# Kernel optimization log

Hardware: AMD Instinct MI355X
Metric: run time of the kernel (lower is better)

## Reference

```python
import jax, jax.numpy as jnp
import numpy as np

EMBED_DIM = 512
NUM_HEADS = 8
HEAD_DIM = EMBED_DIM // NUM_HEADS
B, S = 2, 4096


def setup_inputs() -> dict:
    key = jax.random.key(0)
    ks = jax.random.split(key, 5)
    scale = 1.0 / np.sqrt(EMBED_DIM)
    x = jax.random.normal(ks[0], (B, S, EMBED_DIM), dtype=jnp.float32)
    Wq = jax.random.normal(ks[1], (EMBED_DIM, EMBED_DIM), dtype=jnp.float32) * scale
    Wk = jax.random.normal(ks[2], (EMBED_DIM, EMBED_DIM), dtype=jnp.float32) * scale
    Wv = jax.random.normal(ks[3], (EMBED_DIM, EMBED_DIM), dtype=jnp.float32) * scale
    Wo = jax.random.normal(ks[4], (EMBED_DIM, EMBED_DIM), dtype=jnp.float32) * scale
    z = jnp.zeros((EMBED_DIM,), dtype=jnp.float32)
    return {"x": x, "Wq": Wq, "bq": z, "Wk": Wk, "bk": z, "Wv": Wv, "bv": z, "Wo": Wo, "bo": z}


def _split_heads(t):
    # [B, S, E] -> [B, H, S, Dh]
    b, s, _ = t.shape
    return t.reshape(b, s, NUM_HEADS, HEAD_DIM).transpose(0, 2, 1, 3)


def reference(x, Wq, bq, Wk, bk, Wv, bv, Wo, bo):
    q = _split_heads(x @ Wq + bq)
    k = _split_heads(x @ Wk + bk)
    v = _split_heads(x @ Wv + bv)
    # scaled dot-product attention; scale by sqrt(d_head) as in source
    scores = jnp.einsum("bhqd,bhkd->bhqk", q, k) / jnp.sqrt(jnp.float32(HEAD_DIM))
    weights = jax.nn.softmax(scores, axis=-1)
    attn = jnp.einsum("bhqk,bhkd->bhqd", weights, v)
    concat = attn.transpose(0, 2, 1, 3).reshape(x.shape[0], x.shape[1], EMBED_DIM)
    return concat @ Wo + bo
```

## Files before the change

kernel.cpp:

```cpp
#include <hip/hip_runtime.h>
#include <stdint.h>


typedef __bf16 bf16_t;
typedef bf16_t bf16x8 __attribute__((ext_vector_type(8)));
typedef float f32x4 __attribute__((ext_vector_type(4)));
typedef unsigned short u16;
typedef unsigned int u32;

__device__ __forceinline__ u16 f2bf(float f) {
  return __builtin_bit_cast(u16, (bf16_t)f);
}

__device__ __forceinline__ void gll16(const void* g, void* l) {
  __builtin_amdgcn_global_load_lds((__attribute__((address_space(1))) void*)(void*)(g),
                                   (__attribute__((address_space(3))) void*)(l), 16, 0, 0);
}

__device__ __forceinline__ float fexp2(float x) {
  float r; asm("v_exp_f32 %0, %1" : "=v"(r) : "v"(x)); return r;
}
__device__ __forceinline__ u32 cvtpk(float lo, float hi) {
  u32 r; asm("v_cvt_pk_bf16_f32 %0, %1, %2" : "=v"(r) : "v"(lo), "v"(hi)); return r;
}

__global__ void k_convert(const float* __restrict__ x, u16* __restrict__ xb, int n4) {
  int i = blockIdx.x * blockDim.x + threadIdx.x;
  if (i >= n4) return;
  float4 v = ((const float4*)x)[i];
  ushort4 o;
  o.x = f2bf(v.x); o.y = f2bf(v.y); o.z = f2bf(v.z); o.w = f2bf(v.w);
  ((ushort4*)xb)[i] = o;
}

__global__ void k_transposeW(const float* __restrict__ W0, const float* __restrict__ W1,
                             const float* __restrict__ W2, const float* __restrict__ W3,
                             u16* __restrict__ Wt) {
  __shared__ float tile[64][65];
  const float* W = (blockIdx.z == 0) ? W0 : (blockIdx.z == 1) ? W1 : (blockIdx.z == 2) ? W2 : W3;
  u16* out = Wt + (size_t)blockIdx.z * (512 * 512);
  int k0 = blockIdx.x * 64, n0 = blockIdx.y * 64;
  int t = threadIdx.x;
#pragma unroll
  for (int i = 0; i < 16; ++i) {
    int idx = i * 256 + t;
    int r = idx >> 6, c = idx & 63;
    tile[r][c] = W[(size_t)(k0 + r) * 512 + n0 + c];
  }
  __syncthreads();
#pragma unroll
  for (int i = 0; i < 16; ++i) {
    int idx = i * 256 + t;
    int n = idx >> 6, k = idx & 63;
    out[(size_t)(n0 + n) * 512 + k0 + k] = f2bf(tile[k][n]);
  }
}

__device__ __forceinline__ void gemm_core(const u16* __restrict__ A, const u16* __restrict__ Bt,
                                          int m0, int n0, uint8_t* lds, f32x4 (&acc)[4][4]) {
  int t = threadIdx.x;
  int lane = t & 63;
  int wid = t >> 6;
  int l15 = lane & 15, hib = (lane >> 4) * 16;
  int wm = wid >> 1, wn = wid & 1;
  const uint8_t* Ab = (const uint8_t*)A + (size_t)m0 * 1024;
  const uint8_t* Bb = (const uint8_t*)Bt + (size_t)n0 * 1024;
  for (int kk = 0; kk < 8; ++kk) {
    __syncthreads();
    int kof = kk * 128;
#pragma unroll
    for (int r = 0; r < 4; ++r) {
      int L = r * 4096 + t * 16;
      int row = L >> 7;
      int colU = (L & 127) ^ ((row & 7) << 4);
      gll16(Ab + (size_t)row * 1024 + kof + colU, lds + L);
      gll16(Bb + (size_t)row * 1024 + kof + colU, lds + 16384 + L);
    }
    __syncthreads();
#pragma unroll
    for (int ks = 0; ks < 2; ++ks) {
      bf16x8 af[4], bfr[4];
#pragma unroll
      for (int mi = 0; mi < 4; ++mi) {
        int row = wm * 64 + mi * 16 + l15;
        af[mi] = *(const bf16x8*)(lds + row * 128 + ((ks * 64 + hib) ^ ((row & 7) << 4)));
      }
#pragma unroll
      for (int ni = 0; ni < 4; ++ni) {
        int row = wn * 64 + ni * 16 + l15;
        bfr[ni] = *(const bf16x8*)(lds + 16384 + row * 128 + ((ks * 64 + hib) ^ ((row & 7) << 4)));
      }
#pragma unroll
      for (int mi = 0; mi < 4; ++mi)
#pragma unroll
        for (int ni = 0; ni < 4; ++ni)
          acc[mi][ni] = __builtin_amdgcn_mfma_f32_16x16x32_bf16(af[mi], bfr[ni], acc[mi][ni], 0, 0, 0);
    }
  }
  __syncthreads();
}

__global__ __launch_bounds__(256, 2) void k_gemm_qkv(
    const u16* __restrict__ A, const u16* __restrict__ Wt,
    const float* __restrict__ bq, const float* __restrict__ bk, const float* __restrict__ bv,
    u16* __restrict__ Qo, u16* __restrict__ Ko, u16* __restrict__ Vt) {
  __shared__ uint8_t lds[34816];
  int z = blockIdx.z;
  const u16* Bt = Wt + (size_t)z * (512 * 512);
  const float* bias = (z == 0) ? bq : (z == 1) ? bk : bv;
  float qsc = (z == 0) ? 0.18033688011112042f : 1.0f;
  int m0 = blockIdx.y * 128, n0 = blockIdx.x * 128;
  int t = threadIdx.x, lane = t & 63, wid = t >> 6;
  int l15 = lane & 15;
  int wm = wid >> 1, wn = wid & 1;

  f32x4 acc[4][4] = {};
  gemm_core(A, Bt, m0, n0, lds, acc);

  if (z != 2) {
    u16* out = (z == 0) ? Qo : Ko;
#pragma unroll
    for (int mi = 0; mi < 4; ++mi)
#pragma unroll
      for (int ni = 0; ni < 4; ++ni) {
        int c = wn * 64 + ni * 16 + l15;
        float bsv = bias[n0 + c];
        int rbase = wm * 64 + mi * 16 + (lane >> 4) * 4;
#pragma unroll
        for (int i = 0; i < 4; ++i)
          *(u16*)(lds + (rbase + i) * 256 + c * 2) = f2bf((acc[mi][ni][i] + bsv) * qsc);
      }
    __syncthreads();
#pragma unroll
    for (int rr = 0; rr < 8; ++rr) {
      int L = rr * 4096 + t * 16;
      int row = L >> 8, col = L & 255;
      *(uint4*)((uint8_t*)out + (size_t)(m0 + row) * 1024 + n0 * 2 + col) = *(const uint4*)(lds + L);
    }
  } else {
#pragma unroll
    for (int mi = 0; mi < 4; ++mi)
#pragma unroll
      for (int ni = 0; ni < 4; ++ni) {
        int c = wn * 64 + ni * 16 + l15;
        float bsv = bias[n0 + c];
        int rbase = wm * 64 + mi * 16 + (lane >> 4) * 4;
#pragma unroll
        for (int i = 0; i < 4; ++i)
          *(u16*)(lds + c * 272 + (rbase + i) * 2) = f2bf(acc[mi][ni][i] + bsv);
      }
    __syncthreads();
    int b = m0 >> 12, s0 = m0 & 4095;
#pragma unroll
    for (int rr = 0; rr < 8; ++rr) {
      int L = rr * 4096 + t * 16;
      int cidx = L >> 8, rb = L & 255;
      *(uint4*)((uint8_t*)Vt + (size_t)(b * 512 + n0 + cidx) * 8192 + s0 * 2 + rb) =
          *(const uint4*)(lds + cidx * 272 + rb);
    }
  }
}

__global__ __launch_bounds__(256, 2) void k_gemm_out(
    const u16* __restrict__ A, const u16* __restrict__ Bt,
    const float* __restrict__ bias, float* __restrict__ out) {
  __shared__ uint8_t lds[32768];
  int m0 = blockIdx.y * 128, n0 = blockIdx.x * 128;
  int t = threadIdx.x, lane = t & 63, wid = t >> 6;
  int l15 = lane & 15;
  int wm = wid >> 1, wn = wid & 1;

  f32x4 acc[4][4] = {};
  gemm_core(A, Bt, m0, n0, lds, acc);

#pragma unroll
  for (int mi = 0; mi < 4; ++mi)
#pragma unroll
    for (int ni = 0; ni < 4; ++ni) {
      int c = wn * 64 + ni * 16 + l15;
      float bsv = bias[n0 + c];
      int rbase = wm * 64 + mi * 16 + (lane >> 4) * 4;
#pragma unroll
      for (int i = 0; i < 4; ++i)
        out[(size_t)(m0 + rbase + i) * 512 + n0 + c] = acc[mi][ni][i] + bsv;
    }
}

__global__ __launch_bounds__(256, 2) void k_attn(
    const u16* __restrict__ Q, const u16* __restrict__ K,
    const u16* __restrict__ Vt, u16* __restrict__ O) {
  __shared__ uint8_t lds[34816];
  int t = threadIdx.x, lane = t & 63, wid = t >> 6;
  int l15 = lane & 15, hi = lane >> 4;
  int g = wid >> 1, p = wid & 1;
  int bh = blockIdx.y, b = bh >> 3, h = bh & 7;
  int q0 = blockIdx.x * 128 + g * 64;

  const uint8_t* Kbase = (const uint8_t*)K + (size_t)(b * 4096) * 1024 + h * 128;
  const uint8_t* Vbase = (const uint8_t*)Vt + (size_t)(b * 512 + h * 64) * 8192;

  bf16x8 qf[4][2];
#pragma unroll
  for (int qs = 0; qs < 4; ++qs)
#pragma unroll
    for (int ks = 0; ks < 2; ++ks)
      qf[qs][ks] = *(const bf16x8*)(Q + (size_t)(b * 4096 + q0 + qs * 16 + l15) * 512 +
                                    h * 64 + ks * 32 + hi * 8);

  uint4 ou; ou.x = 0x3F803F80u; ou.y = 0x3F803F80u; ou.z = 0x3F803F80u; ou.w = 0x3F803F80u;
  const bf16x8 ones = __builtin_bit_cast(bf16x8, ou);

  f32x4 o[4][4] = {};
  f32x4 oden[4] = {};

  auto STAGE = [&](int buf, int kt) {
    uint8_t* Kl = lds + buf * 16384;
    uint8_t* Vl = Kl + 8192;
    int kv0 = kt * 64;
#pragma unroll
    for (int r = 0; r < 2; ++r) {
      int L = r * 4096 + t * 16;
      int row = L >> 7;
      int colU = (L & 127) ^ ((row & 7) << 4);
      gll16(Kbase + (size_t)(kv0 + row) * 1024 + colU, Kl + L);
      gll16(Vbase + (size_t)row * 8192 + (size_t)kv0 * 2 + colU, Vl + L);
    }
  };

  STAGE(0, 0);
  asm volatile("s_waitcnt vmcnt(0)" ::: "memory");
  __builtin_amdgcn_s_barrier();

  int cur = 0;
  for (int kt = 0; kt < 64; ++kt) {
    if (kt + 1 < 64) STAGE(cur ^ 1, kt + 1);

    const uint8_t* Kl = lds + cur * 16384;
    const uint8_t* Vl = Kl + 8192;

    bf16x8 kA[2][2];
#pragma unroll
    for (int ks = 0; ks < 2; ++ks)
#pragma unroll
      for (int cg = 0; cg < 2; ++cg) {
        int row = p * 32 + cg * 16 + l15;
        kA[ks][cg] = *(const bf16x8*)(Kl + row * 128 + ((ks * 64 + hi * 16) ^ ((row & 7) << 4)));
      }

    f32x4 s[4][2] = {};
    __builtin_amdgcn_s_setprio(1);
#pragma unroll
    for (int qs = 0; qs < 4; ++qs)
#pragma unroll
      for (int ks = 0; ks < 2; ++ks)
#pragma unroll
        for (int cg = 0; cg < 2; ++cg)
          s[qs][cg] = __builtin_amdgcn_mfma_f32_16x16x32_bf16(kA[ks][cg], qf[qs][ks], s[qs][cg], 0, 0, 0);
    __builtin_amdgcn_s_setprio(0);

    bf16x8 pb[4];
#pragma unroll
    for (int qs = 0; qs < 4; ++qs) {
      float pv[8];
#pragma unroll
      for (int cg = 0; cg < 2; ++cg)
#pragma unroll
        for (int i = 0; i < 4; ++i)
          pv[cg * 4 + i] = fexp2(s[qs][cg][i]);
      uint4 pu;
      pu.x = cvtpk(pv[0], pv[1]);
      pu.y = cvtpk(pv[2], pv[3]);
      pu.z = cvtpk(pv[4], pv[5]);
      pu.w = cvtpk(pv[6], pv[7]);
      pb[qs] = __builtin_bit_cast(bf16x8, pu);
    }

    __builtin_amdgcn_s_setprio(1);
#pragma unroll
    for (int qs = 0; qs < 4; ++qs)
      oden[qs] = __builtin_amdgcn_mfma_f32_16x16x32_bf16(ones, pb[qs], oden[qs], 0, 0, 0);
#pragma unroll
    for (int dg = 0; dg < 4; ++dg) {
      int row = dg * 16 + l15;
      int sw = (row & 7) << 4;
      uint2 a0 = *(const uint2*)(Vl + row * 128 + ((p * 64 + hi * 8) ^ sw));
      uint2 a1 = *(const uint2*)(Vl + row * 128 + ((p * 64 + 32 + hi * 8) ^ sw));
      uint4 vv; vv.x = a0.x; vv.y = a0.y; vv.z = a1.x; vv.w = a1.y;
      bf16x8 va = __builtin_bit_cast(bf16x8, vv);
#pragma unroll
      for (int qs = 0; qs < 4; ++qs)
        o[qs][dg] = __builtin_amdgcn_mfma_f32_16x16x32_bf16(va, pb[qs], o[qs][dg], 0, 0, 0);
    }
    __builtin_amdgcn_s_setprio(0);

    asm volatile("s_waitcnt vmcnt(0)" ::: "memory");
    __builtin_amdgcn_s_barrier();
    cur ^= 1;
  }

  float den[4];
#pragma unroll
  for (int qs = 0; qs < 4; ++qs) den[qs] = oden[qs][0];

  uint8_t* base = lds + g * 17408;
  if (p) {
#pragma unroll
    for (int qs = 0; qs < 4; ++qs) {
#pragma unroll
      for (int dg = 0; dg < 4; ++dg)
        *(f32x4*)(base + ((qs * 4 + dg) * 64 + lane) * 16) = o[qs][dg];
      *(float*)(base + 16384 + (qs * 64 + lane) * 4) = den[qs];
    }
  }
  __syncthreads();
  if (!p) {
#pragma unroll
    for (int qs = 0; qs < 4; ++qs) {
      float pl = *(const float*)(base + 16384 + (qs * 64 + lane) * 4);
      float inv = 1.0f / (den[qs] + pl);
#pragma unroll
      for (int dg = 0; dg < 4; ++dg) {
        f32x4 po = *(const f32x4*)(base + ((qs * 4 + dg) * 64 + lane) * 16);
        ushort4 pk;
        pk.x = f2bf((o[qs][dg][0] + po[0]) * inv);
        pk.y = f2bf((o[qs][dg][1] + po[1]) * inv);
        pk.z = f2bf((o[qs][dg][2] + po[2]) * inv);
        pk.w = f2bf((o[qs][dg][3] + po[3]) * inv);
        *(uint2*)(O + (size_t)(b * 4096 + q0 + qs * 16 + l15) * 512 + h * 64 + dg * 16 + hi * 4) =
            __builtin_bit_cast(uint2, pk);
      }
    }
  }
}

extern "C" void kernel_launch(void* const* d_in, const int* in_sizes, int n_in,
                              void* d_out, int out_size, void* d_ws, size_t ws_size,
                              hipStream_t stream) {
  const float* x  = (const float*)d_in[0];
  const float* Wq = (const float*)d_in[1];
  const float* bq = (const float*)d_in[2];
  const float* Wk = (const float*)d_in[3];
  const float* bk = (const float*)d_in[4];
  const float* Wv = (const float*)d_in[5];
  const float* bv = (const float*)d_in[6];
  const float* Wo = (const float*)d_in[7];
  const float* bo = (const float*)d_in[8];
  float* out = (float*)d_out;

  uint8_t* ws = (uint8_t*)d_ws;
  u16* xb  = (u16*)(ws);
  u16* Wt  = (u16*)(ws + 8388608);
  u16* Qb  = (u16*)(ws + 10485760);
  u16* Kb  = (u16*)(ws + 18874368);
  u16* Vtb = (u16*)(ws + 27262976);
  u16* attn = xb;

  k_convert<<<4096, 256, 0, stream>>>(x, xb, 1048576);
  k_transposeW<<<dim3(8, 8, 4), 256, 0, stream>>>(Wq, Wk, Wv, Wo, Wt);
  k_gemm_qkv<<<dim3(4, 64, 3), 256, 0, stream>>>(xb, Wt, bq, bk, bv, Qb, Kb, Vtb);
  k_attn<<<dim3(32, 16), 256, 0, stream>>>(Qb, Kb, Vtb, attn);
  k_gemm_out<<<dim3(4, 64), 256, 0, stream>>>(attn, Wt + 3 * 262144, bo, out);
}
```

Before: 114.9 us.

## Double-buffer GEMM K-loop and widen attention KV stage to 128 rows

```diff
diff --git a/kernel.cpp b/kernel.cpp
--- a/kernel.cpp
+++ b/kernel.cpp
@@ -65,30 +65,42 @@
   int wm = wid >> 1, wn = wid & 1;
   const uint8_t* Ab = (const uint8_t*)A + (size_t)m0 * 1024;
   const uint8_t* Bb = (const uint8_t*)Bt + (size_t)n0 * 1024;
-  for (int kk = 0; kk < 8; ++kk) {
-    __syncthreads();
+
+  auto STAGE = [&](int buf, int kk) {
     int kof = kk * 128;
+    uint8_t* Al = lds + buf * 32768;
+    uint8_t* Bl = Al + 16384;
 #pragma unroll
     for (int r = 0; r < 4; ++r) {
       int L = r * 4096 + t * 16;
       int row = L >> 7;
       int colU = (L & 127) ^ ((row & 7) << 4);
-      gll16(Ab + (size_t)row * 1024 + kof + colU, lds + L);
-      gll16(Bb + (size_t)row * 1024 + kof + colU, lds + 16384 + L);
-    }
-    __syncthreads();
+      gll16(Ab + (size_t)row * 1024 + kof + colU, Al + L);
+      gll16(Bb + (size_t)row * 1024 + kof + colU, Bl + L);
+    }
+  };
+
+  STAGE(0, 0);
+  asm volatile("s_waitcnt vmcnt(0)" ::: "memory");
+  __builtin_amdgcn_s_barrier();
+
+  int cur = 0;
+  for (int kk = 0; kk < 8; ++kk) {
+    if (kk + 1 < 8) STAGE(cur ^ 1, kk + 1);
+    const uint8_t* Al = lds + cur * 32768;
+    const uint8_t* Bl = Al + 16384;
 #pragma unroll
     for (int ks = 0; ks < 2; ++ks) {
       bf16x8 af[4], bfr[4];
 #pragma unroll
       for (int mi = 0; mi < 4; ++mi) {
         int row = wm * 64 + mi * 16 + l15;
-        af[mi] = *(const bf16x8*)(lds + row * 128 + ((ks * 64 + hib) ^ ((row & 7) << 4)));
+        af[mi] = *(const bf16x8*)(Al + row * 128 + ((ks * 64 + hib) ^ ((row & 7) << 4)));
       }
 #pragma unroll
       for (int ni = 0; ni < 4; ++ni) {
         int row = wn * 64 + ni * 16 + l15;
-        bfr[ni] = *(const bf16x8*)(lds + 16384 + row * 128 + ((ks * 64 + hib) ^ ((row & 7) << 4)));
+        bfr[ni] = *(const bf16x8*)(Bl + row * 128 + ((ks * 64 + hib) ^ ((row & 7) << 4)));
       }
 #pragma unroll
       for (int mi = 0; mi < 4; ++mi)
@@ -96,15 +108,17 @@
         for (int ni = 0; ni < 4; ++ni)
           acc[mi][ni] = __builtin_amdgcn_mfma_f32_16x16x32_bf16(af[mi], bfr[ni], acc[mi][ni], 0, 0, 0);
     }
-  }
-  __syncthreads();
+    asm volatile("s_waitcnt vmcnt(0)" ::: "memory");
+    __builtin_amdgcn_s_barrier();
+    cur ^= 1;
+  }
 }
 
 __global__ __launch_bounds__(256, 2) void k_gemm_qkv(
     const u16* __restrict__ A, const u16* __restrict__ Wt,
     const float* __restrict__ bq, const float* __restrict__ bk, const float* __restrict__ bv,
     u16* __restrict__ Qo, u16* __restrict__ Ko, u16* __restrict__ Vt) {
-  __shared__ uint8_t lds[34816];
+  __shared__ uint8_t lds[65536];
   int z = blockIdx.z;
   const u16* Bt = Wt + (size_t)z * (512 * 512);
   const float* bias = (z == 0) ? bq : (z == 1) ? bk : bv;
@@ -164,7 +178,7 @@
 __global__ __launch_bounds__(256, 2) void k_gemm_out(
     const u16* __restrict__ A, const u16* __restrict__ Bt,
     const float* __restrict__ bias, float* __restrict__ out) {
-  __shared__ uint8_t lds[32768];
+  __shared__ uint8_t lds[65536];
   int m0 = blockIdx.y * 128, n0 = blockIdx.x * 128;
   int t = threadIdx.x, lane = t & 63, wid = t >> 6;
   int l15 = lane & 15;
@@ -189,7 +203,7 @@
 __global__ __launch_bounds__(256, 2) void k_attn(
     const u16* __restrict__ Q, const u16* __restrict__ K,
     const u16* __restrict__ Vt, u16* __restrict__ O) {
-  __shared__ uint8_t lds[34816];
+  __shared__ uint8_t lds[65536];
   int t = threadIdx.x, lane = t & 63, wid = t >> 6;
   int l15 = lane & 15, hi = lane >> 4;
   int g = wid >> 1, p = wid & 1;
@@ -213,17 +227,19 @@
   f32x4 o[4][4] = {};
   f32x4 oden[4] = {};
 
-  auto STAGE = [&](int buf, int kt) {
-    uint8_t* Kl = lds + buf * 16384;
-    uint8_t* Vl = Kl + 8192;
-    int kv0 = kt * 64;
-#pragma unroll
-    for (int r = 0; r < 2; ++r) {
+  auto STAGE = [&](int buf, int kt2) {
+    uint8_t* Kl = lds + buf * 32768;
+    uint8_t* Vl = Kl + 16384;
+    int kv0 = kt2 * 128;
+#pragma unroll
+    for (int r = 0; r < 4; ++r) {
       int L = r * 4096 + t * 16;
-      int row = L >> 7;
-      int colU = (L & 127) ^ ((row & 7) << 4);
-      gll16(Kbase + (size_t)(kv0 + row) * 1024 + colU, Kl + L);
-      gll16(Vbase + (size_t)row * 8192 + (size_t)kv0 * 2 + colU, Vl + L);
+      int rowK = L >> 7;
+      int colK = (L & 127) ^ ((rowK & 7) << 4);
+      gll16(Kbase + (size_t)(kv0 + rowK) * 1024 + colK, Kl + L);
+      int rowV = (L >> 7) & 63, sub = L >> 13;
+      int colV = (L & 127) ^ ((rowV & 7) << 4);
+      gll16(Vbase + (size_t)rowV * 8192 + (size_t)(kv0 + sub * 64) * 2 + colV, Vl + L);
     }
   };
 
@@ -232,66 +248,72 @@
   __builtin_amdgcn_s_barrier();
 
   int cur = 0;
-  for (int kt = 0; kt < 64; ++kt) {
-    if (kt + 1 < 64) STAGE(cur ^ 1, kt + 1);
-
-    const uint8_t* Kl = lds + cur * 16384;
-    const uint8_t* Vl = Kl + 8192;
-
-    bf16x8 kA[2][2];
-#pragma unroll
-    for (int ks = 0; ks < 2; ++ks)
-#pragma unroll
-      for (int cg = 0; cg < 2; ++cg) {
-        int row = p * 32 + cg * 16 + l15;
-        kA[ks][cg] = *(const bf16x8*)(Kl + row * 128 + ((ks * 64 + hi * 16) ^ ((row & 7) << 4)));
-      }
-
-    f32x4 s[4][2] = {};
-    __builtin_amdgcn_s_setprio(1);
-#pragma unroll
-    for (int qs = 0; qs < 4; ++qs)
+  for (int kt2 = 0; kt2 < 32; ++kt2) {
+    if (kt2 + 1 < 32) STAGE(cur ^ 1, kt2 + 1);
+
+    uint8_t* Kbuf = lds + cur * 32768;
+    uint8_t* Vbuf = Kbuf + 16384;
+
+#pragma unroll
+    for (int sub = 0; sub < 2; ++sub) {
+      const uint8_t* Kl = Kbuf + sub * 8192;
+      const uint8_t* Vl = Vbuf + sub * 8192;
+
+      bf16x8 kA[2][2];
 #pragma unroll
       for (int ks = 0; ks < 2; ++ks)
 #pragma unroll
+        for (int cg = 0; cg < 2; ++cg) {
+          int row = p * 32 + cg * 16 + l15;
+          kA[ks][cg] = *(const bf16x8*)(Kl + row * 128 + ((ks * 64 + hi * 16) ^ ((row & 7) << 4)));
+        }
+
+      f32x4 s[4][2] = {};
+      __builtin_amdgcn_s_setprio(1);
+#pragma unroll
+      for (int qs = 0; qs < 4; ++qs)
+#pragma unroll
+        for (int ks = 0; ks < 2; ++ks)
+#pragma unroll
+          for (int cg = 0; cg < 2; ++cg)
+            s[qs][cg] = __builtin_amdgcn_mfma_f32_16x16x32_bf16(kA[ks][cg], qf[qs][ks], s[qs][cg], 0, 0, 0);
+      __builtin_amdgcn_s_setprio(0);
+
+      bf16x8 pb[4];
+#pragma unroll
+      for (int qs = 0; qs < 4; ++qs) {
+        float pv[8];
+#pragma unroll
         for (int cg = 0; cg < 2; ++cg)
-          s[qs][cg] = __builtin_amdgcn_mfma_f32_16x16x32_bf16(kA[ks][cg], qf[qs][ks], s[qs][cg], 0, 0, 0);
-    __builtin_amdgcn_s_setprio(0);
-
-    bf16x8 pb[4];
-#pragma unroll
-    for (int qs = 0; qs < 4; ++qs) {
-      float pv[8];
-#pragma unroll
-      for (int cg = 0; cg < 2; ++cg)
-#pragma unroll
-        for (int i = 0; i < 4; ++i)
-          pv[cg * 4 + i] = fexp2(s[qs][cg][i]);
-      uint4 pu;
-      pu.x = cvtpk(pv[0], pv[1]);
-      pu.y = cvtpk(pv[2], pv[3]);
-      pu.z = cvtpk(pv[4], pv[5]);
-      pu.w = cvtpk(pv[6], pv[7]);
-      pb[qs] = __builtin_bit_cast(bf16x8, pu);
-    }
-
-    __builtin_amdgcn_s_setprio(1);
-#pragma unroll
-    for (int qs = 0; qs < 4; ++qs)
-      oden[qs] = __builtin_amdgcn_mfma_f32_16x16x32_bf16(ones, pb[qs], oden[qs], 0, 0, 0);
-#pragma unroll
-    for (int dg = 0; dg < 4; ++dg) {
-      int row = dg * 16 + l15;
-      int sw = (row & 7) << 4;
-      uint2 a0 = *(const uint2*)(Vl + row * 128 + ((p * 64 + hi * 8) ^ sw));
-      uint2 a1 = *(const uint2*)(Vl + row * 128 + ((p * 64 + 32 + hi * 8) ^ sw));
-      uint4 vv; vv.x = a0.x; vv.y = a0.y; vv.z = a1.x; vv.w = a1.y;
-      bf16x8 va = __builtin_bit_cast(bf16x8, vv);
+#pragma unroll
+          for (int i = 0; i < 4; ++i)
+            pv[cg * 4 + i] = fexp2(s[qs][cg][i]);
+        uint4 pu;
+        pu.x = cvtpk(pv[0], pv[1]);
+        pu.y = cvtpk(pv[2], pv[3]);
+        pu.z = cvtpk(pv[4], pv[5]);
+        pu.w = cvtpk(pv[6], pv[7]);
+        pb[qs] = __builtin_bit_cast(bf16x8, pu);
+      }
+
+      __builtin_amdgcn_s_setprio(1);
 #pragma unroll
       for (int qs = 0; qs < 4; ++qs)
-        o[qs][dg] = __builtin_amdgcn_mfma_f32_16x16x32_bf16(va, pb[qs], o[qs][dg], 0, 0, 0);
-    }
-    __builtin_amdgcn_s_setprio(0);
+        oden[qs] = __builtin_amdgcn_mfma_f32_16x16x32_bf16(ones, pb[qs], oden[qs], 0, 0, 0);
+#pragma unroll
+      for (int dg = 0; dg < 4; ++dg) {
+        int row = dg * 16 + l15;
+        int sw = (row & 7) << 4;
+        uint2 a0 = *(const uint2*)(Vl + row * 128 + ((p * 64 + hi * 8) ^ sw));
+        uint2 a1 = *(const uint2*)(Vl + row * 128 + ((p * 64 + 32 + hi * 8) ^ sw));
+        uint4 vv; vv.x = a0.x; vv.y = a0.y; vv.z = a1.x; vv.w = a1.y;
+        bf16x8 va = __builtin_bit_cast(bf16x8, vv);
+#pragma unroll
+        for (int qs = 0; qs < 4; ++qs)
+          o[qs][dg] = __builtin_amdgcn_mfma_f32_16x16x32_bf16(va, pb[qs], o[qs][dg], 0, 0, 0);
+      }
+      __builtin_amdgcn_s_setprio(0);
+    }
 
     asm volatile("s_waitcnt vmcnt(0)" ::: "memory");
     __builtin_amdgcn_s_barrier();
```

Measured after the change: 114.8 us. Within noise of the previous version (-0.1%).
